# Performance work log

Hardware: AMD Instinct MI355X
Metric: run time of the kernel (lower is better)

Reference implementation:

```python
import jax, jax.numpy as jnp
import numpy as np

B, S, H, NH, HD, L, I, M = 2, 2048, 768, 12, 64, 6, 3072, 256
VOCAB, TYPES = 30522, 2
EPS = 1e-6  # layernorm epsilon and FAVOR+ numerical stabilizer


def layer_norm(x, g, b):
    mu = jnp.mean(x, axis=-1, keepdims=True)
    var = jnp.mean(jax.lax.square(x), axis=-1, keepdims=True) - jax.lax.square(mu)
    return (x - mu) * jax.lax.rsqrt(var + EPS) * g + b


def favor_attention(q, k, v, mask, proj):
    # q,k,v: [B,S,NH,HD]; proj: [M,HD] random features; mask: [B,S] float
    dn = 1.0 / np.sqrt(np.sqrt(HD))      # data normalizer for softmax kernel
    ratio = 1.0 / np.sqrt(M)
    qn, kn = q * dn, k * dn
    qp = jnp.einsum('bsnd,md->bsnm', qn, proj)
    kp = jnp.einsum('bsnd,md->bsnm', kn, proj)
    qd = 0.5 * jnp.sum(qn * qn, axis=-1, keepdims=True)
    kd = 0.5 * jnp.sum(kn * kn, axis=-1, keepdims=True)
    # stabilizers: per-position max for queries, global (seq+feature) max for keys
    q_prime = ratio * (jnp.exp(qp - qd - jnp.max(qp, axis=-1, keepdims=True)) + EPS)
    k_prime = ratio * (jnp.exp(kp - kd - jnp.max(kp, axis=(1, 3), keepdims=True)) + EPS)
    k_prime = k_prime * mask[:, :, None, None]
    kv = jnp.einsum('bsnm,bsnd->bnmd', k_prime, v)          # [B,NH,M,HD]
    num = jnp.einsum('bsnm,bnmd->bsnd', q_prime, kv)        # [B,S,NH,HD]
    den = jnp.einsum('bsnm,bnm->bsn', q_prime, jnp.sum(k_prime, axis=1))
    return num / den[..., None]


def setup_inputs() -> dict:
    key = jax.random.key(0)
    ks = jax.random.split(key, 32)
    f = lambda i, shape, s=0.02: (jax.random.normal(ks[i], shape, jnp.float32) * s)
    inp = {
        'input_ids': jax.random.randint(ks[0], (B, S), 0, VOCAB, jnp.int32),
        'token_type_ids': jax.random.randint(ks[1], (B, S), 0, TYPES, jnp.int32),
        'position_ids': jnp.tile(jnp.arange(S, dtype=jnp.int32)[None, :], (B, 1)),
        'attention_mask': jnp.ones((B, S), jnp.int32),
        'word_emb': f(2, (VOCAB, H), 0.1),
        'pos_emb': f(3, (S, H), 0.1),
        'type_emb': f(4, (TYPES, H), 0.1),
        'emb_ln_g': jnp.ones((H,), jnp.float32),
        'emb_ln_b': jnp.zeros((H,), jnp.float32),
        'wq': f(5, (L, H, NH, HD)), 'bq': jnp.zeros((L, NH, HD), jnp.float32),
        'wk': f(6, (L, H, NH, HD)), 'bk': jnp.zeros((L, NH, HD), jnp.float32),
        'wv': f(7, (L, H, NH, HD)), 'bv': jnp.zeros((L, NH, HD), jnp.float32),
        'wo': f(8, (L, NH, HD, H)), 'bo': jnp.zeros((L, H), jnp.float32),
        'ln1_g': jnp.ones((L, H), jnp.float32), 'ln1_b': jnp.zeros((L, H), jnp.float32),
        'wi': f(9, (L, H, I)), 'bi': jnp.zeros((L, I), jnp.float32),
        'wo2': f(10, (L, I, H)), 'bo2': jnp.zeros((L, H), jnp.float32),
        'ln2_g': jnp.ones((L, H), jnp.float32), 'ln2_b': jnp.zeros((L, H), jnp.float32),
        'proj': jax.random.normal(ks[11], (L, M, HD), jnp.float32),
    }
    return inp


def reference(input_ids, token_type_ids, position_ids, attention_mask,
              word_emb, pos_emb, type_emb, emb_ln_g, emb_ln_b,
              wq, bq, wk, bk, wv, bv, wo, bo, ln1_g, ln1_b,
              wi, bi, wo2, bo2, ln2_g, ln2_b, proj):
    mask = attention_mask.astype(jnp.float32)
    x = word_emb[input_ids] + pos_emb[position_ids] + type_emb[token_type_ids]
    x = layer_norm(x, emb_ln_g, emb_ln_b)
    for l in range(L):
        q = jnp.einsum('bsh,hnd->bsnd', x, wq[l]) + bq[l]
        k = jnp.einsum('bsh,hnd->bsnd', x, wk[l]) + bk[l]
        v = jnp.einsum('bsh,hnd->bsnd', x, wv[l]) + bv[l]
        att = favor_attention(q, k, v, mask, proj[l])
        att = jnp.einsum('bsnd,ndh->bsh', att, wo[l]) + bo[l]
        a = layer_norm(att + x, ln1_g[l], ln1_b[l])
        inter = jax.nn.gelu(jnp.einsum('bsh,hi->bsi', a, wi[l]) + bi[l])
        out = jnp.einsum('bsi,ih->bsh', inter, wo2[l]) + bo2[l]
        x = layer_norm(out + a, ln2_g[l], ln2_b[l])
    return x
```

## Files before the change

kernel.cpp:

```cpp
#include <hip/hip_runtime.h>
#include <hip/hip_bf16.h>

#define B_ 2
#define S_ 2048
#define H_ 768
#define NH_ 12
#define HD_ 64
#define L_ 6
#define I_ 3072
#define M_ 256
#define BS_ 4096
#define R_ 49152
#define NXH_ 3145728
#define EPS_ 1e-6f
#define DN_ 0.35355339059327373f
#define RATIO_ 0.0625f

typedef __attribute__((ext_vector_type(8))) short bf16x8;
typedef __attribute__((ext_vector_type(4))) float f32x4;

__device__ __forceinline__ void gload16(const void* g, void* l) {
    __builtin_amdgcn_global_load_lds(
        (const __attribute__((address_space(1))) void*)g,
        (__attribute__((address_space(3))) void*)l, 16, 0, 0);
}

__device__ __forceinline__ float gelu_f(float x) {
    const float c = 0.7978845608028654f;
    float x3 = x * x * x;
    return 0.5f * x * (1.0f + tanhf(c * (x + 0.044715f * x3)));
}

__device__ __forceinline__ void blockReduceSum2(float& a, float& b) {
    __shared__ float sa[4], sb[4];
    int lane = threadIdx.x & 63, wid = threadIdx.x >> 6;
    #pragma unroll
    for (int off = 32; off; off >>= 1) {
        a += __shfl_down(a, off, 64);
        b += __shfl_down(b, off, 64);
    }
    __syncthreads();
    if (lane == 0) { sa[wid] = a; sb[wid] = b; }
    __syncthreads();
    a = sa[0] + sa[1] + sa[2] + sa[3];
    b = sb[0] + sb[1] + sb[2] + sb[3];
    __syncthreads();
}

__device__ __forceinline__ float blockReduceMax(float v) {
    __shared__ float sm[4];
    int lane = threadIdx.x & 63, wid = threadIdx.x >> 6;
    #pragma unroll
    for (int off = 32; off; off >>= 1) v = fmaxf(v, __shfl_down(v, off, 64));
    __syncthreads();
    if (lane == 0) sm[wid] = v;
    __syncthreads();
    float r = fmaxf(fmaxf(sm[0], sm[1]), fmaxf(sm[2], sm[3]));
    __syncthreads();
    return r;
}

template<int ACT, int OUTMODE>
__global__ __launch_bounds__(256) void gemm_pipe3_kernel(
    const __hip_bfloat16* __restrict__ A, const __hip_bfloat16* __restrict__ BT,
    const float* __restrict__ bias, void* __restrict__ Cv,
    int K, int lda, int ldb, int ldc, float* __restrict__ qdkd)
{
    __shared__ __align__(16) unsigned short As[3][128][32];
    __shared__ __align__(16) unsigned short Bs[3][128][32];
    const int tid = threadIdx.x, lane = tid & 63, wid = tid >> 6;
    const int wr = wid >> 1, wc = wid & 1;
    const size_t r0 = (size_t)blockIdx.y * 128;
    const int n0 = blockIdx.x * 128;

    const int srow = lane >> 2;
    const int selem = ((lane & 3) ^ ((srow >> 1) & 3)) * 8;
    const unsigned short* ga0 = (const unsigned short*)A + (r0 + wid * 32 + srow) * (size_t)lda + selem;
    const unsigned short* gb0 = (const unsigned short*)BT + ((size_t)n0 + wid * 32 + srow) * (size_t)ldb + selem;

    f32x4 acc[4][4];
    #pragma unroll
    for (int i = 0; i < 4; i++)
        #pragma unroll
        for (int j = 0; j < 4; j++)
            acc[i][j] = (f32x4){0.f, 0.f, 0.f, 0.f};

    const int lr = lane & 15;
    const int rc8 = (((lane >> 4) ^ ((lr >> 1) & 3))) * 8;

#define STAGE_(t) { const int bb_ = (t) % 3; const int kk_ = (t) * 32;            \
    gload16(ga0 + kk_, &As[bb_][wid * 32][0]);                                    \
    gload16(ga0 + kk_ + 16 * (size_t)lda, &As[bb_][wid * 32 + 16][0]);            \
    gload16(gb0 + kk_, &Bs[bb_][wid * 32][0]);                                    \
    gload16(gb0 + kk_ + 16 * (size_t)ldb, &Bs[bb_][wid * 32 + 16][0]); }

#define ITER_(t, VMSTR, DOSTAGE) {                                                \
    if (DOSTAGE) STAGE_((t) + 2);                                                 \
    asm volatile("s_waitcnt vmcnt(" VMSTR ")" ::: "memory");                      \
    __builtin_amdgcn_sched_barrier(0);                                            \
    __builtin_amdgcn_s_barrier();                                                 \
    __builtin_amdgcn_sched_barrier(0);                                            \
    const int bb_ = (t) % 3;                                                      \
    bf16x8 af[4], bfv[4];                                                         \
    _Pragma("unroll") for (int i = 0; i < 4; i++)                                 \
        af[i] = *(const bf16x8*)&As[bb_][wr * 64 + i * 16 + lr][rc8];             \
    _Pragma("unroll") for (int j = 0; j < 4; j++)                                 \
        bfv[j] = *(const bf16x8*)&Bs[bb_][wc * 64 + j * 16 + lr][rc8];            \
    __builtin_amdgcn_s_setprio(1);                                                \
    _Pragma("unroll") for (int i = 0; i < 4; i++)                                 \
        _Pragma("unroll") for (int j = 0; j < 4; j++)                             \
            acc[i][j] = __builtin_amdgcn_mfma_f32_16x16x32_bf16(af[i], bfv[j], acc[i][j], 0, 0, 0); \
    __builtin_amdgcn_s_setprio(0);                                                \
    __builtin_amdgcn_s_barrier();                                                 \
    __builtin_amdgcn_sched_barrier(0); }

    const int nT = K >> 5;
    STAGE_(0); STAGE_(1);
    for (int t = 0; t < nT - 2; ++t) ITER_(t, "8", true);
    ITER_(nT - 2, "4", false);
    ITER_(nT - 1, "0", false);
#undef ITER_
#undef STAGE_

    const int rr = (lane >> 4) * 4;
    const int cc = lane & 15;
    const size_t seg = (size_t)n0 / 768;
    const int colbase = n0 - (int)seg * 768;
    #pragma unroll
    for (int i = 0; i < 4; i++) {
        #pragma unroll
        for (int rg = 0; rg < 4; rg++) {
            size_t row = r0 + wr * 64 + i * 16 + rr + rg;
            float ss = 0.f;
            #pragma unroll
            for (int j = 0; j < 4; j++) {
                int colw = wc * 64 + j * 16 + cc;
                size_t col = (size_t)n0 + colw;
                float bv_ = bias ? bias[col] : 0.f;
                float v = acc[i][j][rg] + bv_;
                if (ACT == 1) v = gelu_f(v);
                __hip_bfloat16 hb = __float2bfloat16(v);
                if (OUTMODE == 1)
                    ((__hip_bfloat16*)Cv)[row * (size_t)ldc + col] = hb;
                else
                    ((__hip_bfloat16*)Cv)[seg * (size_t)NXH_ + row * 768 + colbase + colw] = hb;
                if (OUTMODE == 2) {
                    float vr = __bfloat162float(hb);
                    ss += vr * vr;
                }
            }
            if (OUTMODE == 2) {
                #pragma unroll
                for (int off = 1; off <= 8; off <<= 1)
                    ss += __shfl_xor(ss, off, 64);
                if (seg < 2 && (lane & 15) == 0) {
                    int nh = colbase / 64 + wc;
                    qdkd[seg * (size_t)R_ + row * 12 + nh] = 0.5f * DN_ * DN_ * ss;
                }
            }
        }
    }
}

__global__ __launch_bounds__(256) void gemm_pipe3_n64_kernel(
    const __hip_bfloat16* __restrict__ A, const __hip_bfloat16* __restrict__ BT,
    const float* __restrict__ bias, float* __restrict__ C,
    int K, int lda, int ldb, int ldc)
{
    __shared__ __align__(16) unsigned short As[3][128][32];
    __shared__ __align__(16) unsigned short Bs[3][64][32];
    const int tid = threadIdx.x, lane = tid & 63, wid = tid >> 6;
    const size_t r0 = (size_t)blockIdx.y * 128;
    const int n0 = blockIdx.x * 64;

    const int srow = lane >> 2;
    const int selem = ((lane & 3) ^ ((srow >> 1) & 3)) * 8;
    const unsigned short* ga0 = (const unsigned short*)A + (r0 + wid * 32 + srow) * (size_t)lda + selem;
    const unsigned short* gb0 = (const unsigned short*)BT + ((size_t)n0 + wid * 16 + srow) * (size_t)ldb + selem;

    f32x4 acc[2][4];
    #pragma unroll
    for (int i = 0; i < 2; i++)
        #pragma unroll
        for (int j = 0; j < 4; j++)
            acc[i][j] = (f32x4){0.f, 0.f, 0.f, 0.f};

    const int lr = lane & 15;
    const int rc8 = (((lane >> 4) ^ ((lr >> 1) & 3))) * 8;

#define STAGE_(t) { const int bb_ = (t) % 3; const int kk_ = (t) * 32;            \
    gload16(ga0 + kk_, &As[bb_][wid * 32][0]);                                    \
    gload16(ga0 + kk_ + 16 * (size_t)lda, &As[bb_][wid * 32 + 16][0]);            \
    gload16(gb0 + kk_, &Bs[bb_][wid * 16][0]); }

#define ITER_(t, VMSTR, DOSTAGE) {                                                \
    if (DOSTAGE) STAGE_((t) + 2);                                                 \
    asm volatile("s_waitcnt vmcnt(" VMSTR ")" ::: "memory");                      \
    __builtin_amdgcn_sched_barrier(0);                                            \
    __builtin_amdgcn_s_barrier();                                                 \
    __builtin_amdgcn_sched_barrier(0);                                            \
    const int bb_ = (t) % 3;                                                      \
    bf16x8 af[2], bfv[4];                                                         \
    _Pragma("unroll") for (int i = 0; i < 2; i++)                                 \
        af[i] = *(const bf16x8*)&As[bb_][wid * 32 + i * 16 + lr][rc8];            \
    _Pragma("unroll") for (int j = 0; j < 4; j++)                                 \
        bfv[j] = *(const bf16x8*)&Bs[bb_][j * 16 + lr][rc8];                      \
    __builtin_amdgcn_s_setprio(1);                                                \
    _Pragma("unroll") for (int i = 0; i < 2; i++)                                 \
        _Pragma("unroll") for (int j = 0; j < 4; j++)                             \
            acc[i][j] = __builtin_amdgcn_mfma_f32_16x16x32_bf16(af[i], bfv[j], acc[i][j], 0, 0, 0); \
    __builtin_amdgcn_s_setprio(0);                                                \
    __builtin_amdgcn_s_barrier();                                                 \
    __builtin_amdgcn_sched_barrier(0); }

    const int nT = K >> 5;
    STAGE_(0); STAGE_(1);
    for (int t = 0; t < nT - 2; ++t) ITER_(t, "6", true);
    ITER_(nT - 2, "3", false);
    ITER_(nT - 1, "0", false);
#undef ITER_
#undef STAGE_

    const int rr = (lane >> 4) * 4, cc = lane & 15;
    #pragma unroll
    for (int i = 0; i < 2; i++) {
        #pragma unroll
        for (int j = 0; j < 4; j++) {
            int col = n0 + j * 16 + cc;
            float bv_ = bias ? bias[col] : 0.f;
            #pragma unroll
            for (int rg = 0; rg < 4; rg++) {
                size_t row = r0 + wid * 32 + i * 16 + rr + rg;
                C[row * (size_t)ldc + col] = acc[i][j][rg] + bv_;
            }
        }
    }
}

__global__ __launch_bounds__(256) void gemm_projk_kernel(
    const __hip_bfloat16* __restrict__ A, const __hip_bfloat16* __restrict__ BT,
    __hip_bfloat16* __restrict__ Cv,
    int K, int lda, int ldb, int ldc, float alpha,
    float* __restrict__ rmaxp)
{
    __shared__ __align__(16) unsigned short As[2][128][32];
    __shared__ __align__(16) unsigned short Bs[2][128][32];
    __shared__ float rmx[128][2];
    const int tid = threadIdx.x, lane = tid & 63, wid = tid >> 6;
    const int wr = wid >> 1, wc = wid & 1;
    const size_t r0 = (size_t)blockIdx.y * 128;
    const int n0 = blockIdx.x * 128;

    const int srow = lane >> 2;
    const int selem = ((lane & 3) ^ ((srow >> 1) & 3)) * 8;
    const unsigned short* ga0 = (const unsigned short*)A + (r0 + wid * 32 + srow) * (size_t)lda + selem;
    const unsigned short* gb0 = (const unsigned short*)BT + ((size_t)n0 + wid * 32 + srow) * (size_t)ldb + selem;

    f32x4 acc[4][4];
    #pragma unroll
    for (int i = 0; i < 4; i++)
        #pragma unroll
        for (int j = 0; j < 4; j++)
            acc[i][j] = (f32x4){0.f, 0.f, 0.f, 0.f};

    gload16(ga0, &As[0][wid * 32][0]);
    gload16(ga0 + 16 * (size_t)lda, &As[0][wid * 32 + 16][0]);
    gload16(gb0, &Bs[0][wid * 32][0]);
    gload16(gb0 + 16 * (size_t)ldb, &Bs[0][wid * 32 + 16][0]);
    __syncthreads();

    const int lr = lane & 15;
    const int rc8 = (((lane >> 4) ^ ((lr >> 1) & 3))) * 8;

    int cur = 0;
    for (int k0 = 0; k0 < K; k0 += 32) {
        const int kn = k0 + 32;
        if (kn < K) {
            gload16(ga0 + kn, &As[cur ^ 1][wid * 32][0]);
            gload16(ga0 + kn + 16 * (size_t)lda, &As[cur ^ 1][wid * 32 + 16][0]);
            gload16(gb0 + kn, &Bs[cur ^ 1][wid * 32][0]);
            gload16(gb0 + kn + 16 * (size_t)ldb, &Bs[cur ^ 1][wid * 32 + 16][0]);
        }
        bf16x8 af[4], bfv[4];
        #pragma unroll
        for (int i = 0; i < 4; i++)
            af[i] = *(const bf16x8*)&As[cur][wr * 64 + i * 16 + lr][rc8];
        #pragma unroll
        for (int j = 0; j < 4; j++)
            bfv[j] = *(const bf16x8*)&Bs[cur][wc * 64 + j * 16 + lr][rc8];
        #pragma unroll
        for (int i = 0; i < 4; i++)
            #pragma unroll
            for (int j = 0; j < 4; j++)
                acc[i][j] = __builtin_amdgcn_mfma_f32_16x16x32_bf16(af[i], bfv[j], acc[i][j], 0, 0, 0);
        __syncthreads();
        cur ^= 1;
    }

    const int rr = (lane >> 4) * 4;
    const int cc = lane & 15;
    #pragma unroll
    for (int i = 0; i < 4; i++) {
        #pragma unroll
        for (int j = 0; j < 4; j++) {
            int colw = wc * 64 + j * 16 + cc;
            size_t col = (size_t)n0 + colw;
            #pragma unroll
            for (int rg = 0; rg < 4; rg++) {
                size_t row = r0 + wr * 64 + i * 16 + rr + rg;
                Cv[row * ldc + col] = __float2bfloat16(acc[i][j][rg] * alpha);
            }
        }
    }
    #pragma unroll
    for (int i = 0; i < 4; i++) {
        #pragma unroll
        for (int rg = 0; rg < 4; rg++) {
            float rm = -3.4e38f;
            #pragma unroll
            for (int j = 0; j < 4; j++) rm = fmaxf(rm, acc[i][j][rg] * alpha);
            #pragma unroll
            for (int off = 1; off <= 8; off <<= 1)
                rm = fmaxf(rm, __shfl_xor(rm, off, 64));
            if ((lane & 15) == 0) rmx[wr * 64 + i * 16 + rr + rg][wc] = rm;
        }
    }
    __syncthreads();
    if (tid < 128)
        rmaxp[(size_t)blockIdx.x * R_ + r0 + tid] = fmaxf(rmx[tid][0], rmx[tid][1]);
}

__global__ __launch_bounds__(512) void projq_den_kernel(
    const __hip_bfloat16* __restrict__ Qbp, const __hip_bfloat16* __restrict__ projb,
    const float* __restrict__ qd, const float* __restrict__ ksum,
    __hip_bfloat16* __restrict__ QPb, float* __restrict__ den)
{
    __shared__ __align__(16) unsigned short Asm[128][64];
    __shared__ __align__(16) unsigned short Bsm[256][64];
    __shared__ float ksl[12][256];
    __shared__ float red[128][4];
    __shared__ float rmaxv[128];
    __shared__ float qdl[128];
    const int tid = threadIdx.x, lane = tid & 63, w = tid >> 6;
    const int wrow = w >> 2, wcol = w & 3;
    const size_t r0 = (size_t)blockIdx.x * 128;
    const int b = (int)(r0 / 24576);

    #pragma unroll
    for (int it = 0; it < 6; it++) {
        int idx = tid + it * 512;
        ksl[idx >> 8][idx & 255] = ksum[((size_t)b * 12 + (idx >> 8)) * 256 + (idx & 255)];
    }
    if (tid < 128) qdl[tid] = qd[r0 + tid];

    const int lrow = lane >> 3, lch = lane & 7;
    const int sch = (lch ^ (lrow & 7)) * 8;
    #pragma unroll
    for (int it = 0; it < 2; it++) {
        int segr = (w * 2 + it) * 8;
        gload16((const unsigned short*)Qbp + (r0 + segr + lrow) * 64 + sch, &Asm[segr][0]);
    }
    #pragma unroll
    for (int it = 0; it < 4; it++) {
        int segr = (w * 4 + it) * 8;
        gload16((const unsigned short*)projb + (size_t)(segr + lrow) * 64 + sch, &Bsm[segr][0]);
    }
    __syncthreads();

    const int lr = lane & 15, kq = lane >> 4;
    f32x4 acc[4][4];
    #pragma unroll
    for (int i = 0; i < 4; i++)
        #pragma unroll
        for (int j = 0; j < 4; j++)
            acc[i][j] = (f32x4){0.f, 0.f, 0.f, 0.f};

    #pragma unroll
    for (int ks = 0; ks < 2; ks++) {
        const int ch = (((ks << 2) | kq) ^ (lr & 7)) * 8;
        bf16x8 af[4], bfv[4];
        #pragma unroll
        for (int i = 0; i < 4; i++)
            af[i] = *(const bf16x8*)&Asm[wrow * 64 + i * 16 + lr][ch];
        #pragma unroll
        for (int j = 0; j < 4; j++)
            bfv[j] = *(const bf16x8*)&Bsm[wcol * 64 + j * 16 + lr][ch];
        #pragma unroll
        for (int i = 0; i < 4; i++)
            #pragma unroll
            for (int j = 0; j < 4; j++)
                acc[i][j] = __builtin_amdgcn_mfma_f32_16x16x32_bf16(af[i], bfv[j], acc[i][j], 0, 0, 0);
    }

    #pragma unroll
    for (int i = 0; i < 4; i++) {
        #pragma unroll
        for (int rg = 0; rg < 4; rg++) {
            float rm = -3.4e38f;
            #pragma unroll
            for (int j = 0; j < 4; j++) rm = fmaxf(rm, acc[i][j][rg] * DN_);
            #pragma unroll
            for (int off = 1; off <= 8; off <<= 1)
                rm = fmaxf(rm, __shfl_xor(rm, off, 64));
            if ((lane & 15) == 0) red[wrow * 64 + i * 16 + kq * 4 + rg][wcol] = rm;
        }
    }
    __syncthreads();
    if (tid < 128)
        rmaxv[tid] = fmaxf(fmaxf(red[tid][0], red[tid][1]), fmaxf(red[tid][2], red[tid][3]));
    __syncthreads();

    #pragma unroll
    for (int i = 0; i < 4; i++) {
        #pragma unroll
        for (int rg = 0; rg < 4; rg++) {
            int row = wrow * 64 + i * 16 + kq * 4 + rg;
            size_t rglob = r0 + row;
            int nh = (int)(rglob % 12);
            float qdv = qdl[row], mx = rmaxv[row];
            float dsum = 0.f;
            #pragma unroll
            for (int j = 0; j < 4; j++) {
                int col = wcol * 64 + j * 16 + lr;
                float qp = acc[i][j][rg] * DN_;
                float qv = RATIO_ * (expf(qp - qdv - mx) + EPS_);
                __hip_bfloat16 qb = __float2bfloat16(qv);
                QPb[rglob * 256 + col] = qb;
                dsum += __bfloat162float(qb) * ksl[nh][col];
            }
            #pragma unroll
            for (int off = 1; off <= 8; off <<= 1)
                dsum += __shfl_xor(dsum, off, 64);
            if ((lane & 15) == 0) red[row][wcol] = dsum;
        }
    }
    __syncthreads();
    if (tid < 128)
        den[r0 + tid] = red[tid][0] + red[tid][1] + red[tid][2] + red[tid][3];
}

__global__ __launch_bounds__(256) void num_mfma_kernel(
    const __hip_bfloat16* __restrict__ QPb, const __hip_bfloat16* __restrict__ kvT,
    const float* __restrict__ den, __hip_bfloat16* __restrict__ ATT)
{
    __shared__ __align__(16) unsigned short As[2][128][32];
    __shared__ __align__(16) unsigned short Bs[2][64][32];
    const int tid = threadIdx.x, lane = tid & 63, wid = tid >> 6;
    const int s0 = blockIdx.x * 128;
    const int bn = blockIdx.y, b = bn / NH_, n = bn % NH_;

    const int srow = lane >> 2;
    const int selem = ((lane & 3) ^ ((srow >> 1) & 3)) * 8;
    const unsigned short* ga0 = (const unsigned short*)QPb + (size_t)b * S_ * (NH_ * M_) + n * M_
                              + ((size_t)s0 + wid * 32 + srow) * (NH_ * M_) + selem;
    const unsigned short* gb0 = (const unsigned short*)kvT + (size_t)bn * (HD_ * M_)
                              + ((size_t)wid * 16 + srow) * M_ + selem;

    f32x4 acc[2][4];
    #pragma unroll
    for (int i = 0; i < 2; i++)
        #pragma unroll
        for (int j = 0; j < 4; j++)
            acc[i][j] = (f32x4){0.f, 0.f, 0.f, 0.f};

    gload16(ga0, &As[0][wid * 32][0]);
    gload16(ga0 + 16 * (size_t)(NH_ * M_), &As[0][wid * 32 + 16][0]);
    gload16(gb0, &Bs[0][wid * 16][0]);
    __syncthreads();

    const int lr = lane & 15;
    const int rc8 = (((lane >> 4) ^ ((lr >> 1) & 3))) * 8;

    int cur = 0;
    for (int k0 = 0; k0 < M_; k0 += 32) {
        const int kn = k0 + 32;
        if (kn < M_) {
            gload16(ga0 + kn, &As[cur ^ 1][wid * 32][0]);
            gload16(ga0 + kn + 16 * (size_t)(NH_ * M_), &As[cur ^ 1][wid * 32 + 16][0]);
            gload16(gb0 + kn, &Bs[cur ^ 1][wid * 16][0]);
        }
        bf16x8 af[2], bfv[4];
        #pragma unroll
        for (int i = 0; i < 2; i++)
            af[i] = *(const bf16x8*)&As[cur][wid * 32 + i * 16 + lr][rc8];
        #pragma unroll
        for (int j = 0; j < 4; j++)
            bfv[j] = *(const bf16x8*)&Bs[cur][j * 16 + lr][rc8];
        #pragma unroll
        for (int i = 0; i < 2; i++)
            #pragma unroll
            for (int j = 0; j < 4; j++)
                acc[i][j] = __builtin_amdgcn_mfma_f32_16x16x32_bf16(af[i], bfv[j], acc[i][j], 0, 0, 0);
        __syncthreads();
        cur ^= 1;
    }

    const int rr = (lane >> 4) * 4, cc = lane & 15;
    #pragma unroll
    for (int i = 0; i < 2; i++) {
        #pragma unroll
        for (int rg = 0; rg < 4; rg++) {
            int s = s0 + wid * 32 + i * 16 + rr + rg;
            float inv = 1.0f / den[((size_t)b * S_ + s) * NH_ + n];
            #pragma unroll
            for (int j = 0; j < 4; j++)
                ATT[((size_t)b * S_ + s) * H_ + n * HD_ + j * 16 + cc]
                    = __float2bfloat16(acc[i][j][rg] * inv);
        }
    }
}

__global__ __launch_bounds__(256) void kv_splitk_kernel(
    const __hip_bfloat16* __restrict__ KPb, const __hip_bfloat16* __restrict__ Vb,
    float* __restrict__ part)
{
    const int m0 = blockIdx.x * 64, bn = blockIdx.y, b = bn / NH_, n = bn % NH_;
    const int s0 = blockIdx.z * 256;
    __shared__ __align__(16) float As2[16][68];
    __shared__ __align__(16) float Bs2[16][68];
    const int tid = threadIdx.x, tx = tid & 15, ty = tid >> 4;
    float acc[4][4] = {};
    for (int ss = 0; ss < 256; ss += 16) {
        #pragma unroll
        for (int i = 0; i < 4; i++) {
            int idx = tid + i * 256;
            int kk = idx >> 6, c = idx & 63;
            size_t srow = (size_t)b * S_ + s0 + ss + kk;
            As2[kk][c] = __bfloat162float(KPb[srow * (NH_ * M_) + n * M_ + m0 + c]);
            Bs2[kk][c] = __bfloat162float(Vb[srow * H_ + n * HD_ + c]);
        }
        __syncthreads();
        #pragma unroll
        for (int kk = 0; kk < 16; kk++) {
            float4 av = *reinterpret_cast<const float4*>(&As2[kk][ty * 4]);
            float4 bv = *reinterpret_cast<const float4*>(&Bs2[kk][tx * 4]);
            float a4[4] = {av.x, av.y, av.z, av.w};
            float b4[4] = {bv.x, bv.y, bv.z, bv.w};
            #pragma unroll
            for (int i = 0; i < 4; i++)
                #pragma unroll
                for (int j = 0; j < 4; j++)
                    acc[i][j] += a4[i] * b4[j];
        }
        __syncthreads();
    }
    float* Cb = part + ((size_t)blockIdx.z * (B_ * NH_) + bn) * (M_ * HD_);
    #pragma unroll
    for (int i = 0; i < 4; i++)
        #pragma unroll
        for (int j = 0; j < 4; j++)
            Cb[(size_t)(m0 + ty * 4 + i) * HD_ + tx * 4 + j] = acc[i][j];
}

__global__ __launch_bounds__(256) void kvred_kernel(
    const float* __restrict__ part, __hip_bfloat16* __restrict__ kvT)
{
    const int bn = blockIdx.x, m = threadIdx.x;
    for (int d = 0; d < HD_; d++) {
        float s = 0.f;
        #pragma unroll
        for (int c = 0; c < 8; c++)
            s += part[((size_t)c * (B_ * NH_) + bn) * (M_ * HD_) + (size_t)m * HD_ + d];
        kvT[(size_t)bn * (HD_ * M_) + (size_t)d * M_ + m] = __float2bfloat16(s);
    }
}

__global__ __launch_bounds__(256) void prep_kernel(
    const float* __restrict__ wq_l, const float* __restrict__ wk_l,
    const float* __restrict__ wv_l, const float* __restrict__ wo_l,
    const float* __restrict__ wi_l, const float* __restrict__ wo2_l,
    const float* __restrict__ proj_l,
    const float* __restrict__ bq_l, const float* __restrict__ bk_l, const float* __restrict__ bv_l,
    __hip_bfloat16* __restrict__ wqT, __hip_bfloat16* __restrict__ wkT,
    __hip_bfloat16* __restrict__ wvT, __hip_bfloat16* __restrict__ woT,
    __hip_bfloat16* __restrict__ wiT, __hip_bfloat16* __restrict__ wo2T,
    __hip_bfloat16* __restrict__ projb, float* __restrict__ biasq)
{
    __shared__ float tile[32][33];
    int bid = blockIdx.x;
    if (bid < 6912) {
        const float* src; __hip_bfloat16* dst; int K, N, kt, nt;
        if (bid < 2304) {
            int t = bid / 576, idx = bid % 576;
            src = (t == 0) ? wq_l : (t == 1) ? wk_l : (t == 2) ? wv_l : wo_l;
            dst = (t == 0) ? wqT : (t == 1) ? wkT : (t == 2) ? wvT : woT;
            K = 768; N = 768; kt = idx % 24; nt = idx / 24;
        } else if (bid < 4608) {
            int idx = bid - 2304;
            src = wi_l; dst = wiT; K = 768; N = 3072;
            kt = idx % 24; nt = idx / 24;
        } else {
            int idx = bid - 4608;
            src = wo2_l; dst = wo2T; K = 3072; N = 768;
            kt = idx % 96; nt = idx / 96;
        }
        int k0 = kt * 32, n0 = nt * 32;
        int tx = threadIdx.x & 31, ty = threadIdx.x >> 5;
        #pragma unroll
        for (int i = 0; i < 4; i++)
            tile[ty + i * 8][tx] = src[(size_t)(k0 + ty + i * 8) * N + n0 + tx];
        __syncthreads();
        #pragma unroll
        for (int i = 0; i < 4; i++)
            dst[(size_t)(n0 + ty + i * 8) * K + k0 + tx] = __float2bfloat16(tile[tx][ty + i * 8]);
    } else if (bid < 6976) {
        int i = (bid - 6912) * 256 + threadIdx.x;
        projb[i] = __float2bfloat16(proj_l[i]);
    } else {
        int i = (bid - 6976) * 256 + threadIdx.x;
        if (i < 768) biasq[i] = bq_l[i];
        else if (i < 1536) biasq[i] = bk_l[i - 768];
        else if (i < 2304) biasq[i] = bv_l[i - 1536];
    }
}

__global__ __launch_bounds__(256) void embed_ln_kernel(
    const int* __restrict__ ids, const int* __restrict__ tts, const int* __restrict__ pos,
    const float* __restrict__ wemb, const float* __restrict__ pemb, const float* __restrict__ temb,
    const float* __restrict__ g, const float* __restrict__ bb,
    float* __restrict__ out, __hip_bfloat16* __restrict__ outb)
{
    size_t row = blockIdx.x;
    int id = ids[row], tt = tts[row], ps = pos[row];
    const float* w0 = wemb + (size_t)id * H_;
    const float* p0 = pemb + (size_t)ps * H_;
    const float* t0 = temb + (size_t)tt * H_;
    float vals[3], s1 = 0.f, s2 = 0.f;
    #pragma unroll
    for (int i = 0; i < 3; i++) {
        int h = threadIdx.x + i * 256;
        float v = w0[h] + p0[h] + t0[h];
        vals[i] = v; s1 += v; s2 += v * v;
    }
    blockReduceSum2(s1, s2);
    float mu = s1 * (1.0f / H_);
    float var = s2 * (1.0f / H_) - mu * mu;
    float rs = rsqrtf(var + EPS_);
    #pragma unroll
    for (int i = 0; i < 3; i++) {
        int h = threadIdx.x + i * 256;
        float y = (vals[i] - mu) * rs * g[h] + bb[h];
        out[row * H_ + h] = y;
        outb[row * H_ + h] = __float2bfloat16(y);
    }
}

__global__ __launch_bounds__(256) void add_ln_kernel(
    const float* __restrict__ P, const float* __restrict__ Q,
    const float* __restrict__ g, const float* __restrict__ bb,
    float* __restrict__ out, __hip_bfloat16* __restrict__ outb)
{
    size_t row = blockIdx.x;
    float vals[3], s1 = 0.f, s2 = 0.f;
    #pragma unroll
    for (int i = 0; i < 3; i++) {
        int h = threadIdx.x + i * 256;
        float v = P[row * H_ + h] + Q[row * H_ + h];
        vals[i] = v; s1 += v; s2 += v * v;
    }
    blockReduceSum2(s1, s2);
    float mu = s1 * (1.0f / H_);
    float var = s2 * (1.0f / H_) - mu * mu;
    float rs = rsqrtf(var + EPS_);
    #pragma unroll
    for (int i = 0; i < 3; i++) {
        int h = threadIdx.x + i * 256;
        float y = (vals[i] - mu) * rs * g[h] + bb[h];
        out[row * H_ + h] = y;
        if (outb) outb[row * H_ + h] = __float2bfloat16(y);
    }
}

__global__ __launch_bounds__(256) void gmax_kernel(
    const float* __restrict__ rmaxp, float* __restrict__ gmax)
{
    int bn = blockIdx.x, b = bn / NH_, n = bn % NH_;
    float mx = -3.4e38f;
    for (int s = threadIdx.x; s < S_; s += 256) {
        size_t r = ((size_t)b * S_ + s) * NH_ + n;
        mx = fmaxf(mx, fmaxf(rmaxp[r], rmaxp[R_ + r]));
    }
    mx = blockReduceMax(mx);
    if (threadIdx.x == 0) gmax[bn] = mx;
}

__global__ __launch_bounds__(256) void kprime_ksum_kernel(
    __hip_bfloat16* __restrict__ KPb, const float* __restrict__ kd,
    const float* __restrict__ gmax, const int* __restrict__ amask,
    float* __restrict__ kpart)
{
    const int bn = blockIdx.x, chunk = blockIdx.y;
    const int b = bn / NH_, n = bn % NH_;
    const int m = threadIdx.x;
    const float gm = gmax[bn];
    float acc = 0.f;
    for (int si = 0; si < 64; si++) {
        size_t bs = (size_t)b * S_ + chunk * 64 + si;
        size_t r = bs * NH_ + n;
        float mk = (float)amask[bs];
        size_t e = r * M_ + m;
        float v = RATIO_ * (expf(__bfloat162float(KPb[e]) - kd[r] - gm) + EPS_) * mk;
        __hip_bfloat16 hb = __float2bfloat16(v);
        KPb[e] = hb;
        acc += __bfloat162float(hb);
    }
    kpart[((size_t)bn * 32 + chunk) * M_ + m] = acc;
}

__global__ __launch_bounds__(256) void ksum_final_kernel(
    const float* __restrict__ part, float* __restrict__ ksum)
{
    int bn = blockIdx.x, m = threadIdx.x;
    float s = 0.f;
    #pragma unroll
    for (int c = 0; c < 32; c++) s += part[((size_t)bn * 32 + c) * M_ + m];
    ksum[(size_t)bn * M_ + m] = s;
}

extern "C" void kernel_launch(void* const* d_in, const int* in_sizes, int n_in,
                              void* d_out, int out_size, void* d_ws, size_t ws_size,
                              hipStream_t stream)
{
    const int* input_ids  = (const int*)d_in[0];
    const int* token_type = (const int*)d_in[1];
    const int* position   = (const int*)d_in[2];
    const int* amask      = (const int*)d_in[3];
    const float* wemb = (const float*)d_in[4];
    const float* pemb = (const float*)d_in[5];
    const float* temb = (const float*)d_in[6];
    const float* elng = (const float*)d_in[7];
    const float* elnb = (const float*)d_in[8];
    const float* wq  = (const float*)d_in[9];
    const float* bq  = (const float*)d_in[10];
    const float* wk  = (const float*)d_in[11];
    const float* bk  = (const float*)d_in[12];
    const float* wv  = (const float*)d_in[13];
    const float* bv  = (const float*)d_in[14];
    const float* wo  = (const float*)d_in[15];
    const float* bo  = (const float*)d_in[16];
    const float* ln1g = (const float*)d_in[17];
    const float* ln1b = (const float*)d_in[18];
    const float* wi  = (const float*)d_in[19];
    const float* bi  = (const float*)d_in[20];
    const float* wo2 = (const float*)d_in[21];
    const float* bo2 = (const float*)d_in[22];
    const float* ln2g = (const float*)d_in[23];
    const float* ln2b = (const float*)d_in[24];
    const float* proj = (const float*)d_in[25];

    float* ws = (float*)d_ws;
    float* X    = ws;
    float* T2   = X + 3145728;
    float* BIG  = T2 + 3145728;
    float* U    = BIG + 12582912;
    __hip_bfloat16* Xb  = (__hip_bfloat16*)(U + 6291456);
    __hip_bfloat16* Qb  = (__hip_bfloat16*)((float*)Xb + 1572864);
    __hip_bfloat16* Kb  = Qb + 3145728;
    __hip_bfloat16* Vb  = Kb + 3145728;
    __hip_bfloat16* BF1 = Vb + 3145728;
    __hip_bfloat16* WT  = BF1 + 3145728;
    float* kvT_f = (float*)(WT + 7094272);
    __hip_bfloat16* kvT = (__hip_bfloat16*)kvT_f;
    float* KSUM  = kvT_f + 196608;
    float* KPART = KSUM + 6144;
    float* RMAXP = KPART + 196608;
    float* GMAX  = RMAXP + 98304;
    float* QD    = GMAX + 64;
    float* KD    = QD + 49152;
    float* DEN   = KD + 49152;
    float* BIASQ = DEN + 49152;
    float* T1    = (float*)d_out;

    __hip_bfloat16* wqT  = WT;
    __hip_bfloat16* wkT  = wqT + 589824;
    __hip_bfloat16* wvT  = wkT + 589824;
    __hip_bfloat16* woT  = wvT + 589824;
    __hip_bfloat16* wiT  = woT + 589824;
    __hip_bfloat16* wo2T = wiT + 2359296;
    __hip_bfloat16* projb = wo2T + 2359296;
    __hip_bfloat16* QPb = (__hip_bfloat16*)U;
    float* PART = U;
    __hip_bfloat16* BIGb = (__hip_bfloat16*)BIG;

    embed_ln_kernel<<<BS_, 256, 0, stream>>>(input_ids, token_type, position,
        wemb, pemb, temb, elng, elnb, X, Xb);

    for (int l = 0; l < L_; l++) {
        const float* wq_l = wq + (size_t)l * H_ * NH_ * HD_;
        const float* wk_l = wk + (size_t)l * H_ * NH_ * HD_;
        const float* wv_l = wv + (size_t)l * H_ * NH_ * HD_;
        const float* wo_l = wo + (size_t)l * NH_ * HD_ * H_;
        const float* bq_l = bq + (size_t)l * NH_ * HD_;
        const float* bk_l = bk + (size_t)l * NH_ * HD_;
        const float* bv_l = bv + (size_t)l * NH_ * HD_;
        const float* bo_l = bo + (size_t)l * H_;
        const float* wi_l = wi + (size_t)l * H_ * I_;
        const float* bi_l = bi + (size_t)l * I_;
        const float* wo2_l = wo2 + (size_t)l * I_ * H_;
        const float* bo2_l = bo2 + (size_t)l * H_;
        const float* proj_l = proj + (size_t)l * M_ * HD_;

        prep_kernel<<<6985, 256, 0, stream>>>(wq_l, wk_l, wv_l, wo_l, wi_l, wo2_l, proj_l,
            bq_l, bk_l, bv_l, wqT, wkT, wvT, woT, wiT, wo2T, projb, BIASQ);

        gemm_pipe3_kernel<0,2><<<dim3(18,32), 256, 0, stream>>>(
            Xb, wqT, BIASQ, (void*)Qb, 768, 768, 768, 768, QD);

        gemm_projk_kernel<<<dim3(2,384), 256, 0, stream>>>(
            Kb, projb, BIGb, 64, 64, 64, 256, DN_, RMAXP);
        gmax_kernel<<<B_*NH_, 256, 0, stream>>>(RMAXP, GMAX);
        kprime_ksum_kernel<<<dim3(B_*NH_, 32), 256, 0, stream>>>(BIGb, KD, GMAX, amask, KPART);
        ksum_final_kernel<<<B_*NH_, 256, 0, stream>>>(KPART, KSUM);
        kv_splitk_kernel<<<dim3(4, B_*NH_, 8), 256, 0, stream>>>(BIGb, Vb, PART);
        kvred_kernel<<<B_*NH_, 256, 0, stream>>>(PART, kvT);

        projq_den_kernel<<<384, 512, 0, stream>>>(Qb, projb, QD, KSUM, QPb, DEN);
        num_mfma_kernel<<<dim3(16, B_*NH_), 256, 0, stream>>>(QPb, kvT, DEN, BF1);

        gemm_pipe3_n64_kernel<<<dim3(12,32), 256, 0, stream>>>(
            BF1, woT, bo_l, T1, 768, 768, 768, 768);
        add_ln_kernel<<<BS_, 256, 0, stream>>>(T1, X, ln1g + (size_t)l*H_, ln1b + (size_t)l*H_, T2, BF1);

        gemm_pipe3_kernel<1,1><<<dim3(24,32), 256, 0, stream>>>(
            BF1, wiT, bi_l, (void*)BIGb, 768, 768, 768, 3072, nullptr);

        gemm_pipe3_n64_kernel<<<dim3(12,32), 256, 0, stream>>>(
            BIGb, wo2T, bo2_l, T1, 3072, 3072, 3072, 768);
        float* xout = (l == L_ - 1) ? (float*)d_out : X;
        add_ln_kernel<<<BS_, 256, 0, stream>>>(T1, T2, ln2g + (size_t)l*H_, ln2b + (size_t)l*H_, xout, Xb);
    }
}
```

Before: 1.881 ms.

## Fuse k-prime into KV kernel and split-K the FFN down-projection

The separate k-prime/ksum pass, which rewrote the projected keys in place, is removed. The KV split-K kernel now computes exp(kp - kd - gmax) with the mask on the fly and accumulates the key sums itself, which saves a full read-write of the large K-feature buffer. The FFN output GEMM moves from the 64-wide-N kernel to the 128x128 pipelined GEMM with 2-way split-K writing fp32 partial planes. A new add_ln3 kernel sums the planes, bias and residual before layernorm. The KV partial layout is transposed and kvred is parallelised over d, at the cost of extra exp work repeated across blocks and fp32 plane traffic.

New measurement: 1.685 ms. 1.12x faster.

```diff
diff --git a/kernel.cpp b/kernel.cpp
--- a/kernel.cpp
+++ b/kernel.cpp
@@ -64,7 +64,7 @@
 __global__ __launch_bounds__(256) void gemm_pipe3_kernel(
     const __hip_bfloat16* __restrict__ A, const __hip_bfloat16* __restrict__ BT,
     const float* __restrict__ bias, void* __restrict__ Cv,
-    int K, int lda, int ldb, int ldc, float* __restrict__ qdkd)
+    int K, int lda, int ldb, int ldc, float* __restrict__ aux)
 {
     __shared__ __align__(16) unsigned short As[3][128][32];
     __shared__ __align__(16) unsigned short Bs[3][128][32];
@@ -72,11 +72,12 @@
     const int wr = wid >> 1, wc = wid & 1;
     const size_t r0 = (size_t)blockIdx.y * 128;
     const int n0 = blockIdx.x * 128;
+    const size_t kbase = (size_t)blockIdx.z * (size_t)K;
 
     const int srow = lane >> 2;
     const int selem = ((lane & 3) ^ ((srow >> 1) & 3)) * 8;
-    const unsigned short* ga0 = (const unsigned short*)A + (r0 + wid * 32 + srow) * (size_t)lda + selem;
-    const unsigned short* gb0 = (const unsigned short*)BT + ((size_t)n0 + wid * 32 + srow) * (size_t)ldb + selem;
+    const unsigned short* ga0 = (const unsigned short*)A + (r0 + wid * 32 + srow) * (size_t)lda + kbase + selem;
+    const unsigned short* gb0 = (const unsigned short*)BT + ((size_t)n0 + wid * 32 + srow) * (size_t)ldb + kbase + selem;
 
     f32x4 acc[4][4];
     #pragma unroll
@@ -124,38 +125,62 @@
 
     const int rr = (lane >> 4) * 4;
     const int cc = lane & 15;
-    const size_t seg = (size_t)n0 / 768;
-    const int colbase = n0 - (int)seg * 768;
-    #pragma unroll
-    for (int i = 0; i < 4; i++) {
-        #pragma unroll
-        for (int rg = 0; rg < 4; rg++) {
-            size_t row = r0 + wr * 64 + i * 16 + rr + rg;
-            float ss = 0.f;
+    if (OUTMODE == 3) {
+        float* fpl = aux + (size_t)blockIdx.z * NXH_;
+        #pragma unroll
+        for (int i = 0; i < 4; i++) {
             #pragma unroll
             for (int j = 0; j < 4; j++) {
-                int colw = wc * 64 + j * 16 + cc;
-                size_t col = (size_t)n0 + colw;
+                size_t col = (size_t)n0 + wc * 64 + j * 16 + cc;
+                #pragma unroll
+                for (int rg = 0; rg < 4; rg++) {
+                    size_t row = r0 + wr * 64 + i * 16 + rr + rg;
+                    fpl[row * (size_t)ldc + col] = acc[i][j][rg];
+                }
+            }
+        }
+    } else if (OUTMODE == 1) {
+        #pragma unroll
+        for (int i = 0; i < 4; i++) {
+            #pragma unroll
+            for (int j = 0; j < 4; j++) {
+                size_t col = (size_t)n0 + wc * 64 + j * 16 + cc;
                 float bv_ = bias ? bias[col] : 0.f;
-                float v = acc[i][j][rg] + bv_;
-                if (ACT == 1) v = gelu_f(v);
-                __hip_bfloat16 hb = __float2bfloat16(v);
-                if (OUTMODE == 1)
-                    ((__hip_bfloat16*)Cv)[row * (size_t)ldc + col] = hb;
-                else
+                #pragma unroll
+                for (int rg = 0; rg < 4; rg++) {
+                    size_t row = r0 + wr * 64 + i * 16 + rr + rg;
+                    float v = acc[i][j][rg] + bv_;
+                    if (ACT == 1) v = gelu_f(v);
+                    ((__hip_bfloat16*)Cv)[row * (size_t)ldc + col] = __float2bfloat16(v);
+                }
+            }
+        }
+    } else {
+        const size_t seg = (size_t)n0 / 768;
+        const int colbase = n0 - (int)seg * 768;
+        #pragma unroll
+        for (int i = 0; i < 4; i++) {
+            #pragma unroll
+            for (int rg = 0; rg < 4; rg++) {
+                size_t row = r0 + wr * 64 + i * 16 + rr + rg;
+                float ss = 0.f;
+                #pragma unroll
+                for (int j = 0; j < 4; j++) {
+                    int colw = wc * 64 + j * 16 + cc;
+                    size_t col = (size_t)n0 + colw;
+                    float bv_ = bias ? bias[col] : 0.f;
+                    float v = acc[i][j][rg] + bv_;
+                    __hip_bfloat16 hb = __float2bfloat16(v);
                     ((__hip_bfloat16*)Cv)[seg * (size_t)NXH_ + row * 768 + colbase + colw] = hb;
-                if (OUTMODE == 2) {
                     float vr = __bfloat162float(hb);
                     ss += vr * vr;
                 }
-            }
-            if (OUTMODE == 2) {
                 #pragma unroll
                 for (int off = 1; off <= 8; off <<= 1)
                     ss += __shfl_xor(ss, off, 64);
                 if (seg < 2 && (lane & 15) == 0) {
                     int nh = colbase / 64 + wc;
-                    qdkd[seg * (size_t)R_ + row * 12 + nh] = 0.5f * DN_ * DN_ * ss;
+                    aux[seg * (size_t)R_ + row * 12 + nh] = 0.5f * DN_ * DN_ * ss;
                 }
             }
         }
@@ -510,23 +535,33 @@
     }
 }
 
-__global__ __launch_bounds__(256) void kv_splitk_kernel(
-    const __hip_bfloat16* __restrict__ KPb, const __hip_bfloat16* __restrict__ Vb,
-    float* __restrict__ part)
+__global__ __launch_bounds__(256) void kv_fused_kernel(
+    const __hip_bfloat16* __restrict__ KF, const __hip_bfloat16* __restrict__ Vb,
+    const float* __restrict__ kd, const float* __restrict__ gmax,
+    const int* __restrict__ amask,
+    float* __restrict__ part, float* __restrict__ kpart)
 {
     const int m0 = blockIdx.x * 64, bn = blockIdx.y, b = bn / NH_, n = bn % NH_;
     const int s0 = blockIdx.z * 256;
     __shared__ __align__(16) float As2[16][68];
     __shared__ __align__(16) float Bs2[16][68];
+    __shared__ float sred[4][64];
     const int tid = threadIdx.x, tx = tid & 15, ty = tid >> 4;
+    const float gm = gmax[bn];
     float acc[4][4] = {};
+    float ks = 0.f;
     for (int ss = 0; ss < 256; ss += 16) {
         #pragma unroll
         for (int i = 0; i < 4; i++) {
             int idx = tid + i * 256;
             int kk = idx >> 6, c = idx & 63;
             size_t srow = (size_t)b * S_ + s0 + ss + kk;
-            As2[kk][c] = __bfloat162float(KPb[srow * (NH_ * M_) + n * M_ + m0 + c]);
+            float kdv = kd[srow * 12 + n];
+            float mk = (float)amask[srow];
+            float kf = __bfloat162float(KF[srow * (NH_ * M_) + n * M_ + m0 + c]);
+            float kp = RATIO_ * (expf(kf - kdv - gm) + EPS_) * mk;
+            As2[kk][c] = kp;
+            ks += kp;
             Bs2[kk][c] = __bfloat162float(Vb[srow * H_ + n * HD_ + c]);
         }
         __syncthreads();
@@ -546,23 +581,26 @@
     }
     float* Cb = part + ((size_t)blockIdx.z * (B_ * NH_) + bn) * (M_ * HD_);
     #pragma unroll
-    for (int i = 0; i < 4; i++)
-        #pragma unroll
-        for (int j = 0; j < 4; j++)
-            Cb[(size_t)(m0 + ty * 4 + i) * HD_ + tx * 4 + j] = acc[i][j];
+    for (int j = 0; j < 4; j++)
+        #pragma unroll
+        for (int i = 0; i < 4; i++)
+            Cb[(size_t)(tx * 4 + j) * M_ + m0 + ty * 4 + i] = acc[i][j];
+    sred[tid >> 6][tid & 63] = ks;
+    __syncthreads();
+    if (tid < 64)
+        kpart[((size_t)bn * 8 + blockIdx.z) * M_ + m0 + tid]
+            = sred[0][tid] + sred[1][tid] + sred[2][tid] + sred[3][tid];
 }
 
 __global__ __launch_bounds__(256) void kvred_kernel(
     const float* __restrict__ part, __hip_bfloat16* __restrict__ kvT)
 {
-    const int bn = blockIdx.x, m = threadIdx.x;
-    for (int d = 0; d < HD_; d++) {
-        float s = 0.f;
-        #pragma unroll
-        for (int c = 0; c < 8; c++)
-            s += part[((size_t)c * (B_ * NH_) + bn) * (M_ * HD_) + (size_t)m * HD_ + d];
-        kvT[(size_t)bn * (HD_ * M_) + (size_t)d * M_ + m] = __float2bfloat16(s);
-    }
+    const int bn = blockIdx.x, d = blockIdx.y, m = threadIdx.x;
+    float s = 0.f;
+    #pragma unroll
+    for (int c = 0; c < 8; c++)
+        s += part[((size_t)c * (B_ * NH_) + bn) * (M_ * HD_) + (size_t)d * M_ + m];
+    kvT[(size_t)bn * (HD_ * M_) + (size_t)d * M_ + m] = __float2bfloat16(s);
 }
 
 __global__ __launch_bounds__(256) void prep_kernel(
@@ -671,6 +709,34 @@
     }
 }
 
+__global__ __launch_bounds__(256) void add_ln3_kernel(
+    const float* __restrict__ planes, const float* __restrict__ bias,
+    const float* __restrict__ Q,
+    const float* __restrict__ g, const float* __restrict__ bb,
+    float* __restrict__ out, __hip_bfloat16* __restrict__ outb)
+{
+    size_t row = blockIdx.x;
+    float vals[3], s1 = 0.f, s2 = 0.f;
+    #pragma unroll
+    for (int i = 0; i < 3; i++) {
+        int h = threadIdx.x + i * 256;
+        size_t e = row * H_ + h;
+        float v = planes[e] + planes[NXH_ + e] + bias[h] + Q[e];
+        vals[i] = v; s1 += v; s2 += v * v;
+    }
+    blockReduceSum2(s1, s2);
+    float mu = s1 * (1.0f / H_);
+    float var = s2 * (1.0f / H_) - mu * mu;
+    float rs = rsqrtf(var + EPS_);
+    #pragma unroll
+    for (int i = 0; i < 3; i++) {
+        int h = threadIdx.x + i * 256;
+        float y = (vals[i] - mu) * rs * g[h] + bb[h];
+        out[row * H_ + h] = y;
+        outb[row * H_ + h] = __float2bfloat16(y);
+    }
+}
+
 __global__ __launch_bounds__(256) void gmax_kernel(
     const float* __restrict__ rmaxp, float* __restrict__ gmax)
 {
@@ -684,36 +750,13 @@
     if (threadIdx.x == 0) gmax[bn] = mx;
 }
 
-__global__ __launch_bounds__(256) void kprime_ksum_kernel(
-    __hip_bfloat16* __restrict__ KPb, const float* __restrict__ kd,
-    const float* __restrict__ gmax, const int* __restrict__ amask,
-    float* __restrict__ kpart)
-{
-    const int bn = blockIdx.x, chunk = blockIdx.y;
-    const int b = bn / NH_, n = bn % NH_;
-    const int m = threadIdx.x;
-    const float gm = gmax[bn];
-    float acc = 0.f;
-    for (int si = 0; si < 64; si++) {
-        size_t bs = (size_t)b * S_ + chunk * 64 + si;
-        size_t r = bs * NH_ + n;
-        float mk = (float)amask[bs];
-        size_t e = r * M_ + m;
-        float v = RATIO_ * (expf(__bfloat162float(KPb[e]) - kd[r] - gm) + EPS_) * mk;
-        __hip_bfloat16 hb = __float2bfloat16(v);
-        KPb[e] = hb;
-        acc += __bfloat162float(hb);
-    }
-    kpart[((size_t)bn * 32 + chunk) * M_ + m] = acc;
-}
-
 __global__ __launch_bounds__(256) void ksum_final_kernel(
     const float* __restrict__ part, float* __restrict__ ksum)
 {
     int bn = blockIdx.x, m = threadIdx.x;
     float s = 0.f;
     #pragma unroll
-    for (int c = 0; c < 32; c++) s += part[((size_t)bn * 32 + c) * M_ + m];
+    for (int c = 0; c < 8; c++) s += part[((size_t)bn * 8 + c) * M_ + m];
     ksum[(size_t)bn * M_ + m] = s;
 }
 
@@ -780,6 +823,7 @@
     __hip_bfloat16* projb = wo2T + 2359296;
     __hip_bfloat16* QPb = (__hip_bfloat16*)U;
     float* PART = U;
+    float* PLANES = U;
     __hip_bfloat16* BIGb = (__hip_bfloat16*)BIG;
 
     embed_ln_kernel<<<BS_, 256, 0, stream>>>(input_ids, token_type, position,
@@ -809,10 +853,10 @@
         gemm_projk_kernel<<<dim3(2,384), 256, 0, stream>>>(
             Kb, projb, BIGb, 64, 64, 64, 256, DN_, RMAXP);
         gmax_kernel<<<B_*NH_, 256, 0, stream>>>(RMAXP, GMAX);
-        kprime_ksum_kernel<<<dim3(B_*NH_, 32), 256, 0, stream>>>(BIGb, KD, GMAX, amask, KPART);
+        kv_fused_kernel<<<dim3(4, B_*NH_, 8), 256, 0, stream>>>(
+            BIGb, Vb, KD, GMAX, amask, PART, KPART);
         ksum_final_kernel<<<B_*NH_, 256, 0, stream>>>(KPART, KSUM);
-        kv_splitk_kernel<<<dim3(4, B_*NH_, 8), 256, 0, stream>>>(BIGb, Vb, PART);
-        kvred_kernel<<<B_*NH_, 256, 0, stream>>>(PART, kvT);
+        kvred_kernel<<<dim3(B_*NH_, HD_), 256, 0, stream>>>(PART, kvT);
 
         projq_den_kernel<<<384, 512, 0, stream>>>(Qb, projb, QD, KSUM, QPb, DEN);
         num_mfma_kernel<<<dim3(16, B_*NH_), 256, 0, stream>>>(QPb, kvT, DEN, BF1);
@@ -824,9 +868,10 @@
         gemm_pipe3_kernel<1,1><<<dim3(24,32), 256, 0, stream>>>(
             BF1, wiT, bi_l, (void*)BIGb, 768, 768, 768, 3072, nullptr);
 
-        gemm_pipe3_n64_kernel<<<dim3(12,32), 256, 0, stream>>>(
-            BIGb, wo2T, bo2_l, T1, 3072, 3072, 3072, 768);
+        gemm_pipe3_kernel<0,3><<<dim3(6,32,2), 256, 0, stream>>>(
+            BIGb, wo2T, nullptr, nullptr, 1536, 3072, 3072, 768, PLANES);
         float* xout = (l == L_ - 1) ? (float*)d_out : X;
-        add_ln_kernel<<<BS_, 256, 0, stream>>>(T1, T2, ln2g + (size_t)l*H_, ln2b + (size_t)l*H_, xout, Xb);
-    }
-}
+        add_ln3_kernel<<<BS_, 256, 0, stream>>>(PLANES, bo2_l, T2,
+            ln2g + (size_t)l*H_, ln2b + (size_t)l*H_, xout, Xb);
+    }
+}
```
